# Kernel optimization log

Hardware: AMD Instinct MI355X
Metric: run time of the kernel (lower is better)

## Reference

```python
import jax, jax.numpy as jnp
import numpy as np

N_NODES = 50000
N_EDGES = 800000
D_IN = 7
H = 64
STEPS = 3


def _mlp(x, Ws, bs, act):
    n = len(Ws)
    for i in range(n):
        x = x @ Ws[i] + bs[i]
        if i < n - 1:
            x = act(x)
    return x


def _layer_norm(x, scale, bias, eps=1e-6):
    mu = jnp.mean(x, axis=-1, keepdims=True)
    var = jnp.var(x, axis=-1, keepdims=True)
    return (x - mu) * jax.lax.rsqrt(var + eps) * scale + bias


def setup_inputs() -> dict:
    key = jax.random.key(0)
    ks = jax.random.split(key, 32)

    def w(k, shape):
        fan_in = shape[-2] if len(shape) >= 2 else 1
        return jax.random.normal(k, shape, dtype=jnp.float32) / np.sqrt(fan_in)

    inp = {}
    inp["nodes"] = jax.random.normal(ks[0], (N_NODES, D_IN), dtype=jnp.float32)
    inp["senders"] = jax.random.randint(ks[1], (N_EDGES,), 0, N_NODES, dtype=jnp.int32)
    inp["receivers"] = jax.random.randint(ks[2], (N_EDGES,), 0, N_NODES, dtype=jnp.int32)

    inp["W_emb"] = w(ks[3], (D_IN, H))
    inp["b_emb"] = jnp.zeros((H,), jnp.float32)

    # edge MLPs: step 0 first layer sees concat(senders, receivers) = 2H,
    # steps 1,2 see concat(edges, senders, receivers) = 3H; hidden layers H->H
    inp["eW0_first"] = w(ks[4], (2 * H, H))
    inp["eW0_rest"] = w(ks[5], (2, 3 * H, H))
    inp["eW_hid"] = w(ks[6], (STEPS, 2, H, H))
    inp["eb"] = jnp.zeros((STEPS, 3, H), jnp.float32)

    # node MLPs: first layer sees concat(nodes, received) = 2H every step
    inp["nW0"] = w(ks[7], (STEPS, 2 * H, H))
    inp["nW_hid"] = w(ks[8], (STEPS, 2, H, H))
    inp["nb"] = jnp.zeros((STEPS, 3, H), jnp.float32)

    # layer norms per step (nodes and edges)
    inp["ln_ns"] = jnp.ones((STEPS, H), jnp.float32)
    inp["ln_nb"] = jnp.zeros((STEPS, H), jnp.float32)
    inp["ln_es"] = jnp.ones((STEPS, H), jnp.float32)
    inp["ln_eb"] = jnp.zeros((STEPS, H), jnp.float32)

    # readout MLP widths: [4*H, 2*H, 2*H, 1]
    inp["rW1"] = w(ks[9], (H, 4 * H))
    inp["rb1"] = jnp.zeros((4 * H,), jnp.float32)
    inp["rW2"] = w(ks[10], (4 * H, 2 * H))
    inp["rb2"] = jnp.zeros((2 * H,), jnp.float32)
    inp["rW3"] = w(ks[11], (2 * H, 2 * H))
    inp["rb3"] = jnp.zeros((2 * H,), jnp.float32)
    inp["rW4"] = w(ks[12], (2 * H, 1))
    inp["rb4"] = jnp.zeros((1,), jnp.float32)
    return inp


def reference(nodes, senders, receivers, W_emb, b_emb, eW0_first, eW0_rest,
              eW_hid, eb, nW0, nW_hid, nb, ln_ns, ln_nb, ln_es, ln_eb,
              rW1, rb1, rW2, rb2, rW3, rb3, rW4, rb4):
    act = jax.nn.gelu
    x = nodes @ W_emb + b_emb  # [N, H] initial embedding
    edges = None
    for s in range(STEPS):
        sent = x[senders]      # [E, H] gather
        recv = x[receivers]    # [E, H] gather
        if edges is None:
            e_in = jnp.concatenate([sent, recv], axis=1)          # [E, 2H]
            W0 = eW0_first
        else:
            e_in = jnp.concatenate([edges, sent, recv], axis=1)   # [E, 3H]
            W0 = eW0_rest[s - 1]
        edges = _mlp(e_in, [W0, eW_hid[s, 0], eW_hid[s, 1]],
                     [eb[s, 0], eb[s, 1], eb[s, 2]], act)         # [E, H]
        # aggregate edge messages to receiving nodes (segment_sum scatter)
        received = jax.ops.segment_sum(edges, receivers, num_segments=N_NODES)
        n_in = jnp.concatenate([x, received], axis=1)             # [N, 2H]
        x = _mlp(n_in, [nW0[s], nW_hid[s, 0], nW_hid[s, 1]],
                 [nb[s, 0], nb[s, 1], nb[s, 2]], act)             # [N, H]
        x = _layer_norm(x, ln_ns[s], ln_nb[s])
        edges = _layer_norm(edges, ln_es[s], ln_eb[s])
    agg = jnp.mean(x, axis=0)  # graph readout, [H]
    out = _mlp(agg, [rW1, rW2, rW3, rW4], [rb1, rb2, rb3, rb4], act)  # [1]
    return out
```

## Files before the change

### kernel.cpp

```cpp
#include <hip/hip_runtime.h>
#include <hip/hip_bf16.h>


typedef unsigned short ushort;
typedef unsigned int uint;
using bf16x8 = __attribute__((ext_vector_type(8))) short;
using f32x4 = __attribute__((ext_vector_type(4))) float;

__device__ __forceinline__ f32x4 mfma16(bf16x8 a, bf16x8 b, f32x4 c) {
    return __builtin_amdgcn_mfma_f32_16x16x32_bf16(a, b, c, 0, 0, 0);
}

__device__ __forceinline__ ushort f2bf(float x) {
    union { float f; uint u; } v;
    v.f = x;
    uint r = v.u + 0x7fffu + ((v.u >> 16) & 1u);
    return (ushort)(r >> 16);
}
__device__ __forceinline__ float bf2f(ushort u) {
    union { uint u; float f; } v;
    v.u = ((uint)u) << 16;
    return v.f;
}

__device__ __forceinline__ float gelu(float x) {
    float x3 = x * x * x;
    return 0.5f * x * (1.f + tanhf(0.7978845608028654f * (x + 0.044715f * x3)));
}

__device__ __forceinline__ float wave_ln(float v, float lns, float lnb) {
    float s1 = v, s2 = v * v;
#pragma unroll
    for (int m = 32; m; m >>= 1) {
        s1 += __shfl_xor(s1, m, 64);
        s2 += __shfl_xor(s2, m, 64);
    }
    float mu = s1 * (1.f / 64.f);
    float var = s2 * (1.f / 64.f) - mu * mu;
    return (v - mu) * rsqrtf(var + 1e-6f) * lns + lnb;
}

__global__ void k_prep(const float* __restrict__ W, ushort* __restrict__ dh,
                       ushort* __restrict__ dm, ushort* __restrict__ dl,
                       int K) {
    int tid = blockIdx.x * 256 + threadIdx.x;
    if (tid >= K * 64) return;
    int j = tid & 7;
    int lane = (tid >> 3) & 63;
    int hb = (tid >> 9) & 3;
    int kc = tid >> 11;
    int k = kc * 32 + 8 * (lane >> 4) + j;
    int h = hb * 16 + (lane & 15);
    float x = W[k * 64 + h];
    ushort uh = f2bf(x);
    float r = x - bf2f(uh);
    ushort um = f2bf(r);
    float r2 = r - bf2f(um);
    ushort ul = f2bf(r2);
    dh[tid] = uh;
    dm[tid] = um;
    dl[tid] = ul;
}

template <int KC>
__device__ __forceinline__ void mfma_layer(const float* Asrc, int pad,
                                           const ushort* __restrict__ Bh,
                                           const ushort* __restrict__ Bm,
                                           const ushort* __restrict__ Bl,
                                           int lane, f32x4 acc[4]) {
    int e15 = lane & 15, l4 = lane >> 4;
#pragma unroll
    for (int kc = 0; kc < KC; ++kc) {
        const float4* ap =
            reinterpret_cast<const float4*>(Asrc + e15 * pad + kc * 32 + 8 * l4);
        float4 q0 = ap[0];
        float4 q1 = ap[1];
        float av[8] = {q0.x, q0.y, q0.z, q0.w, q1.x, q1.y, q1.z, q1.w};
        bf16x8 ah, am, al;
#pragma unroll
        for (int j = 0; j < 8; ++j) {
            float v = av[j];
            ushort h = f2bf(v);
            float r = v - bf2f(h);
            ushort m = f2bf(r);
            float r2 = r - bf2f(m);
            ushort l = f2bf(r2);
            ah[j] = (short)h;
            am[j] = (short)m;
            al[j] = (short)l;
        }
#pragma unroll
        for (int hb = 0; hb < 4; ++hb) {
            int bi = ((kc * 4 + hb) * 64 + lane) * 8;
            bf16x8 bh_ = *reinterpret_cast<const bf16x8*>(Bh + bi);
            bf16x8 bm_ = *reinterpret_cast<const bf16x8*>(Bm + bi);
            bf16x8 bl_ = *reinterpret_cast<const bf16x8*>(Bl + bi);
            acc[hb] = mfma16(ah, bh_, acc[hb]);
            acc[hb] = mfma16(ah, bm_, acc[hb]);
            acc[hb] = mfma16(am, bh_, acc[hb]);
            acc[hb] = mfma16(ah, bl_, acc[hb]);
            acc[hb] = mfma16(am, bm_, acc[hb]);
            acc[hb] = mfma16(al, bh_, acc[hb]);
        }
    }
}

template <int KIN>
__global__ __launch_bounds__(256) void k_edge_mfma(
    const float* __restrict__ x, float* __restrict__ eraw,
    const int* __restrict__ senders, const int* __restrict__ receivers,
    const ushort* __restrict__ B0h, const ushort* __restrict__ B0m,
    const ushort* __restrict__ B0l, const ushort* __restrict__ B1h,
    const ushort* __restrict__ B1m, const ushort* __restrict__ B1l,
    const ushort* __restrict__ B2h, const ushort* __restrict__ B2m,
    const ushort* __restrict__ B2l, const float* __restrict__ b0,
    const float* __restrict__ b1, const float* __restrict__ b2,
    const float* __restrict__ lnp_s, const float* __restrict__ lnp_b,
    int n_edges) {
    constexpr int KC0 = KIN / 32;
    constexpr int PAD0 = KIN + 8;
    constexpr int PAD1 = 72;
    __shared__ float As[4][16 * PAD0];
    __shared__ float Aa[4][16 * PAD1];
    int tid = threadIdx.x;
    int lane = tid & 63;
    int wsub = tid >> 6;
    float* Aw = As[wsub];
    float* Av = Aa[wsub];
    int e15 = lane & 15, l4 = lane >> 4;

    float plns = 0.f, plnb = 0.f;
    if constexpr (KIN == 192) {
        plns = lnp_s[lane];
        plnb = lnp_b[lane];
    }
    float bv0[4], bv1[4], bv2[4];
#pragma unroll
    for (int hb = 0; hb < 4; ++hb) {
        bv0[hb] = b0[hb * 16 + e15];
        bv1[hb] = b1[hb * 16 + e15];
        bv2[hb] = b2[hb * 16 + e15];
    }

    int wid = blockIdx.x * 4 + wsub;
    int nw = gridDim.x * 4;
    int ntiles = (n_edges + 15) >> 4;

    for (int t = wid; t < ntiles; t += nw) {
        int base = t << 4;
        for (int i = 0; i < 16; ++i) {
            int e = base + i;
            if (e < n_edges) {
                int snd = senders[e];
                int rcv = receivers[e];
                float s = x[(size_t)snd * 64 + lane];
                float r = x[(size_t)rcv * 64 + lane];
                if constexpr (KIN == 192) {
                    float p = wave_ln(eraw[(size_t)e * 64 + lane], plns, plnb);
                    Aw[i * PAD0 + lane] = p;
                    Aw[i * PAD0 + 64 + lane] = s;
                    Aw[i * PAD0 + 128 + lane] = r;
                } else {
                    Aw[i * PAD0 + lane] = s;
                    Aw[i * PAD0 + 64 + lane] = r;
                }
            }
        }
        f32x4 acc[4];
#pragma unroll
        for (int hb = 0; hb < 4; ++hb)
            acc[hb] = (f32x4){bv0[hb], bv0[hb], bv0[hb], bv0[hb]};
        mfma_layer<KC0>(Aw, PAD0, B0h, B0m, B0l, lane, acc);
#pragma unroll
        for (int hb = 0; hb < 4; ++hb)
#pragma unroll
            for (int r = 0; r < 4; ++r)
                Av[(4 * l4 + r) * PAD1 + hb * 16 + e15] = gelu(acc[hb][r]);
#pragma unroll
        for (int hb = 0; hb < 4; ++hb)
            acc[hb] = (f32x4){bv1[hb], bv1[hb], bv1[hb], bv1[hb]};
        mfma_layer<2>(Av, PAD1, B1h, B1m, B1l, lane, acc);
#pragma unroll
        for (int hb = 0; hb < 4; ++hb)
#pragma unroll
            for (int r = 0; r < 4; ++r)
                Av[(4 * l4 + r) * PAD1 + hb * 16 + e15] = gelu(acc[hb][r]);
#pragma unroll
        for (int hb = 0; hb < 4; ++hb)
            acc[hb] = (f32x4){bv2[hb], bv2[hb], bv2[hb], bv2[hb]};
        mfma_layer<2>(Av, PAD1, B2h, B2m, B2l, lane, acc);
#pragma unroll
        for (int hb = 0; hb < 4; ++hb)
#pragma unroll
            for (int r = 0; r < 4; ++r) {
                int e = base + 4 * l4 + r;
                if (e < n_edges)
                    eraw[(size_t)e * 64 + hb * 16 + e15] = acc[hb][r];
            }
    }
}

__global__ __launch_bounds__(256) void k_node_mfma(
    const float* __restrict__ x, const float* __restrict__ eraw,
    const int* __restrict__ row_start, const int* __restrict__ elist,
    const ushort* __restrict__ B0h, const ushort* __restrict__ B0m,
    const ushort* __restrict__ B0l, const ushort* __restrict__ B1h,
    const ushort* __restrict__ B1m, const ushort* __restrict__ B1l,
    const ushort* __restrict__ B2h, const ushort* __restrict__ B2m,
    const ushort* __restrict__ B2l, const float* __restrict__ b0,
    const float* __restrict__ b1, const float* __restrict__ b2,
    const float* __restrict__ ln_s, const float* __restrict__ ln_b,
    float* __restrict__ xout, int n) {
    constexpr int PAD0 = 136;
    constexpr int PAD1 = 72;
    __shared__ float As[4][16 * PAD0];
    __shared__ float Aa[4][16 * PAD1];
    int tid = threadIdx.x;
    int lane = tid & 63;
    int wsub = tid >> 6;
    float* Aw = As[wsub];
    float* Av = Aa[wsub];
    int e15 = lane & 15, l4 = lane >> 4;

    float bv0[4], bv1[4], bv2[4], lnsv[4], lnbv[4];
#pragma unroll
    for (int hb = 0; hb < 4; ++hb) {
        bv0[hb] = b0[hb * 16 + e15];
        bv1[hb] = b1[hb * 16 + e15];
        bv2[hb] = b2[hb * 16 + e15];
        lnsv[hb] = ln_s[hb * 16 + e15];
        lnbv[hb] = ln_b[hb * 16 + e15];
    }

    int wid = blockIdx.x * 4 + wsub;
    int nw = gridDim.x * 4;
    int ntiles = (n + 15) >> 4;

    for (int t = wid; t < ntiles; t += nw) {
        int base = t << 4;
        for (int i = 0; i < 16; ++i) {
            int v = base + i;
            if (v < n) {
                float xv = x[(size_t)v * 64 + lane];
                int i0 = row_start[v], i1 = row_start[v + 1];
                float rv = 0.f, rv2 = 0.f;
                int ii = i0;
                for (; ii + 1 < i1; ii += 2) {
                    rv += eraw[(size_t)elist[ii] * 64 + lane];
                    rv2 += eraw[(size_t)elist[ii + 1] * 64 + lane];
                }
                if (ii < i1) rv += eraw[(size_t)elist[ii] * 64 + lane];
                rv += rv2;
                Aw[i * PAD0 + lane] = xv;
                Aw[i * PAD0 + 64 + lane] = rv;
            }
        }
        f32x4 acc[4];
#pragma unroll
        for (int hb = 0; hb < 4; ++hb)
            acc[hb] = (f32x4){bv0[hb], bv0[hb], bv0[hb], bv0[hb]};
        mfma_layer<4>(Aw, PAD0, B0h, B0m, B0l, lane, acc);
#pragma unroll
        for (int hb = 0; hb < 4; ++hb)
#pragma unroll
            for (int r = 0; r < 4; ++r)
                Av[(4 * l4 + r) * PAD1 + hb * 16 + e15] = gelu(acc[hb][r]);
#pragma unroll
        for (int hb = 0; hb < 4; ++hb)
            acc[hb] = (f32x4){bv1[hb], bv1[hb], bv1[hb], bv1[hb]};
        mfma_layer<2>(Av, PAD1, B1h, B1m, B1l, lane, acc);
#pragma unroll
        for (int hb = 0; hb < 4; ++hb)
#pragma unroll
            for (int r = 0; r < 4; ++r)
                Av[(4 * l4 + r) * PAD1 + hb * 16 + e15] = gelu(acc[hb][r]);
#pragma unroll
        for (int hb = 0; hb < 4; ++hb)
            acc[hb] = (f32x4){bv2[hb], bv2[hb], bv2[hb], bv2[hb]};
        mfma_layer<2>(Av, PAD1, B2h, B2m, B2l, lane, acc);
        float s1[4] = {0.f, 0.f, 0.f, 0.f}, s2[4] = {0.f, 0.f, 0.f, 0.f};
#pragma unroll
        for (int hb = 0; hb < 4; ++hb)
#pragma unroll
            for (int r = 0; r < 4; ++r) {
                float vv = acc[hb][r];
                s1[r] += vv;
                s2[r] += vv * vv;
            }
#pragma unroll
        for (int m = 1; m <= 8; m <<= 1)
#pragma unroll
            for (int r = 0; r < 4; ++r) {
                s1[r] += __shfl_xor(s1[r], m, 64);
                s2[r] += __shfl_xor(s2[r], m, 64);
            }
#pragma unroll
        for (int r = 0; r < 4; ++r) {
            int v = base + 4 * l4 + r;
            if (v < n) {
                float mu = s1[r] * (1.f / 64.f);
                float var = s2[r] * (1.f / 64.f) - mu * mu;
                float rs = rsqrtf(var + 1e-6f);
#pragma unroll
                for (int hb = 0; hb < 4; ++hb)
                    xout[(size_t)v * 64 + hb * 16 + e15] =
                        (acc[hb][r] - mu) * rs * lnsv[hb] + lnbv[hb];
            }
        }
    }
}

__global__ void k_hist(const int* __restrict__ receivers, int* __restrict__ cnt,
                       int nE) {
    int e = blockIdx.x * blockDim.x + threadIdx.x;
    if (e < nE) atomicAdd(&cnt[receivers[e]], 1);
}

__global__ void k_scan1(const int* __restrict__ cnt, int* __restrict__ bsum,
                        int n) {
    __shared__ int sb[256];
    int t = threadIdx.x;
    int i = blockIdx.x * 256 + t;
    sb[t] = (i < n) ? cnt[i] : 0;
    __syncthreads();
    for (int off = 128; off; off >>= 1) {
        if (t < off) sb[t] += sb[t + off];
        __syncthreads();
    }
    if (t == 0) bsum[blockIdx.x] = sb[0];
}

__global__ void k_scan2(int* __restrict__ bsum, int nb) {
    __shared__ int sb[256];
    int t = threadIdx.x;
    int v = (t < nb) ? bsum[t] : 0;
    sb[t] = v;
    __syncthreads();
    for (int off = 1; off < 256; off <<= 1) {
        int add = (t >= off) ? sb[t - off] : 0;
        __syncthreads();
        sb[t] += add;
        __syncthreads();
    }
    if (t < nb) bsum[t] = sb[t] - v;
}

__global__ void k_scan3(const int* __restrict__ cnt, const int* __restrict__ bsum,
                        int* __restrict__ row_start, int* __restrict__ cursor,
                        int n, int nE) {
    __shared__ int sb[256];
    int t = threadIdx.x;
    int i = blockIdx.x * 256 + t;
    int v = (i < n) ? cnt[i] : 0;
    sb[t] = v;
    __syncthreads();
    for (int off = 1; off < 256; off <<= 1) {
        int add = (t >= off) ? sb[t - off] : 0;
        __syncthreads();
        sb[t] += add;
        __syncthreads();
    }
    if (i < n) {
        int ex = bsum[blockIdx.x] + sb[t] - v;
        row_start[i] = ex;
        cursor[i] = ex;
    }
    if (i == n - 1) row_start[n] = nE;
}

__global__ void k_fill(const int* __restrict__ receivers, int* __restrict__ cursor,
                       int* __restrict__ elist, int nE) {
    int e = blockIdx.x * blockDim.x + threadIdx.x;
    if (e < nE) {
        int r = receivers[e];
        int p = atomicAdd(&cursor[r], 1);
        elist[p] = e;
    }
}

__global__ void k_embed(const float* __restrict__ nodes,
                        const float* __restrict__ W, const float* __restrict__ b,
                        float* __restrict__ x, int n) {
    int lane = threadIdx.x & 63;
    int wid = blockIdx.x * 4 + (threadIdx.x >> 6);
    int nw = gridDim.x * 4;
    float wcol[7];
#pragma unroll
    for (int k = 0; k < 7; ++k) wcol[k] = W[k * 64 + lane];
    float bh = b[lane];
    for (int v = wid; v < n; v += nw) {
        float acc = bh;
#pragma unroll
        for (int k = 0; k < 7; ++k) acc = fmaf(nodes[v * 7 + k], wcol[k], acc);
        x[(size_t)v * 64 + lane] = acc;
    }
}

__global__ void k_mean(const float* __restrict__ x, float* __restrict__ agg,
                       int n) {
    int t = threadIdx.x;
    int h = t & 63;
    int sub = t >> 6;
    float s = 0.f;
    for (int v = blockIdx.x * 4 + sub; v < n; v += gridDim.x * 4)
        s += x[(size_t)v * 64 + h];
    __shared__ float buf[256];
    buf[t] = s;
    __syncthreads();
    if (t < 64) {
        float tot = buf[t] + buf[t + 64] + buf[t + 128] + buf[t + 192];
        atomicAdd(&agg[h], tot);
    }
}

__global__ void k_readout(const float* __restrict__ agg,
                          const float* __restrict__ W1, const float* __restrict__ b1,
                          const float* __restrict__ W2, const float* __restrict__ b2,
                          const float* __restrict__ W3, const float* __restrict__ b3,
                          const float* __restrict__ W4, const float* __restrict__ b4,
                          float* __restrict__ out, float inv_n) {
    __shared__ float sA[64], sH1[256], sH2[128], sH3[128];
    int t = threadIdx.x;
    if (t < 64) sA[t] = agg[t] * inv_n;
    __syncthreads();
    {
        float acc = b1[t];
#pragma unroll
        for (int k = 0; k < 64; ++k) acc = fmaf(sA[k], W1[k * 256 + t], acc);
        sH1[t] = gelu(acc);
    }
    __syncthreads();
    if (t < 128) {
        float acc = b2[t];
        for (int k = 0; k < 256; ++k) acc = fmaf(sH1[k], W2[k * 128 + t], acc);
        sH2[t] = gelu(acc);
    }
    __syncthreads();
    if (t < 128) {
        float acc = b3[t];
        for (int k = 0; k < 128; ++k) acc = fmaf(sH2[k], W3[k * 128 + t], acc);
        sH3[t] = gelu(acc);
    }
    __syncthreads();
    if (t < 64) {
        float p = fmaf(sH3[t], W4[t], sH3[t + 64] * W4[t + 64]);
#pragma unroll
        for (int m = 32; m; m >>= 1) p += __shfl_xor(p, m, 64);
        if (t == 0) out[0] = p + b4[0];
    }
}

extern "C" void kernel_launch(void* const* d_in, const int* in_sizes, int n_in,
                              void* d_out, int out_size, void* d_ws,
                              size_t ws_size, hipStream_t stream) {
    const float* nodes = (const float*)d_in[0];
    const int* senders = (const int*)d_in[1];
    const int* receivers = (const int*)d_in[2];
    const float* W_emb = (const float*)d_in[3];
    const float* b_emb = (const float*)d_in[4];
    const float* eW0_first = (const float*)d_in[5];
    const float* eW0_rest = (const float*)d_in[6];
    const float* eW_hid = (const float*)d_in[7];
    const float* eb = (const float*)d_in[8];
    const float* nW0 = (const float*)d_in[9];
    const float* nW_hid = (const float*)d_in[10];
    const float* nb = (const float*)d_in[11];
    const float* ln_ns = (const float*)d_in[12];
    const float* ln_nb = (const float*)d_in[13];
    const float* ln_es = (const float*)d_in[14];
    const float* ln_eb = (const float*)d_in[15];
    const float* rW1 = (const float*)d_in[16];
    const float* rb1 = (const float*)d_in[17];
    const float* rW2 = (const float*)d_in[18];
    const float* rb2 = (const float*)d_in[19];
    const float* rW3 = (const float*)d_in[20];
    const float* rb3 = (const float*)d_in[21];
    const float* rW4 = (const float*)d_in[22];
    const float* rb4 = (const float*)d_in[23];

    const int N = in_sizes[0] / 7;
    const int E = in_sizes[1];

    float* ws = (float*)d_ws;
    float* eraw = ws;
    float* xa = eraw + (size_t)E * 64;
    float* xb = xa + (size_t)N * 64;
    float* agg = xb + (size_t)N * 64;
    int* cnt = (int*)(agg + 64);
    int* row_start = cnt + N;
    int* cursor = row_start + N + 1;
    int* elist = cursor + N;
    int* bsum = elist + E;
    const int WTOT = 106496;
    ushort* wfh = (ushort*)(bsum + 256);
    ushort* wfm = wfh + WTOT;
    ushort* wfl = wfm + WTOT;

    const int OFF_E0 = 0;
    const int OFF_E1 = 8192;
    const int OFF_E2 = 20480;
    const int OFF_EH = 32768;
    const int OFF_N0 = 57344;
    const int OFF_NH = 81920;

    k_prep<<<32, 256, 0, stream>>>(eW0_first, wfh + OFF_E0, wfm + OFF_E0,
                                   wfl + OFF_E0, 128);
    k_prep<<<48, 256, 0, stream>>>(eW0_rest, wfh + OFF_E1, wfm + OFF_E1,
                                   wfl + OFF_E1, 192);
    k_prep<<<48, 256, 0, stream>>>(eW0_rest + (size_t)192 * 64, wfh + OFF_E2,
                                   wfm + OFF_E2, wfl + OFF_E2, 192);
    for (int i = 0; i < 6; ++i) {
        k_prep<<<16, 256, 0, stream>>>(eW_hid + (size_t)i * 4096,
                                       wfh + OFF_EH + i * 4096,
                                       wfm + OFF_EH + i * 4096,
                                       wfl + OFF_EH + i * 4096, 64);
        k_prep<<<16, 256, 0, stream>>>(nW_hid + (size_t)i * 4096,
                                       wfh + OFF_NH + i * 4096,
                                       wfm + OFF_NH + i * 4096,
                                       wfl + OFF_NH + i * 4096, 64);
    }
    for (int s = 0; s < 3; ++s)
        k_prep<<<32, 256, 0, stream>>>(nW0 + (size_t)s * 8192,
                                       wfh + OFF_N0 + s * 8192,
                                       wfm + OFF_N0 + s * 8192,
                                       wfl + OFF_N0 + s * 8192, 128);

    const int nb_scan = (N + 255) / 256;

    hipMemsetAsync(cnt, 0, (size_t)N * sizeof(int), stream);
    k_hist<<<(E + 255) / 256, 256, 0, stream>>>(receivers, cnt, E);
    k_scan1<<<nb_scan, 256, 0, stream>>>(cnt, bsum, N);
    k_scan2<<<1, 256, 0, stream>>>(bsum, nb_scan);
    k_scan3<<<nb_scan, 256, 0, stream>>>(cnt, bsum, row_start, cursor, N, E);
    k_fill<<<(E + 255) / 256, 256, 0, stream>>>(receivers, cursor, elist, E);

    k_embed<<<512, 256, 0, stream>>>(nodes, W_emb, b_emb, xa, N);

    float* xc = xa;
    float* xn = xb;
    for (int s = 0; s < 3; ++s) {
        int h1 = OFF_EH + (s * 2 + 0) * 4096;
        int h2 = OFF_EH + (s * 2 + 1) * 4096;
        const float* eb0 = eb + (s * 3 + 0) * 64;
        const float* eb1 = eb + (s * 3 + 1) * 64;
        const float* eb2 = eb + (s * 3 + 2) * 64;
        if (s == 0) {
            k_edge_mfma<128><<<1024, 256, 0, stream>>>(
                xc, eraw, senders, receivers, wfh + OFF_E0, wfm + OFF_E0,
                wfl + OFF_E0, wfh + h1, wfm + h1, wfl + h1, wfh + h2, wfm + h2,
                wfl + h2, eb0, eb1, eb2, nullptr, nullptr, E);
        } else {
            int w0 = (s == 1) ? OFF_E1 : OFF_E2;
            k_edge_mfma<192><<<1024, 256, 0, stream>>>(
                xc, eraw, senders, receivers, wfh + w0, wfm + w0, wfl + w0,
                wfh + h1, wfm + h1, wfl + h1, wfh + h2, wfm + h2, wfl + h2,
                eb0, eb1, eb2, ln_es + (s - 1) * 64, ln_eb + (s - 1) * 64, E);
        }
        int n1 = OFF_NH + (s * 2 + 0) * 4096;
        int n2 = OFF_NH + (s * 2 + 1) * 4096;
        int n0 = OFF_N0 + s * 8192;
        k_node_mfma<<<512, 256, 0, stream>>>(
            xc, eraw, row_start, elist, wfh + n0, wfm + n0, wfl + n0, wfh + n1,
            wfm + n1, wfl + n1, wfh + n2, wfm + n2, wfl + n2,
            nb + (s * 3 + 0) * 64, nb + (s * 3 + 1) * 64, nb + (s * 3 + 2) * 64,
            ln_ns + s * 64, ln_nb + s * 64, xn, N);
        float* tmp = xc;
        xc = xn;
        xn = tmp;
    }

    hipMemsetAsync(agg, 0, 64 * sizeof(float), stream);
    k_mean<<<256, 256, 0, stream>>>(xc, agg, N);
    k_readout<<<1, 256, 0, stream>>>(agg, rW1, rb1, rW2, rb2, rW3, rb3, rW4,
                                     rb4, (float*)d_out, 1.0f / (float)N);
}
```

Baseline: 4.220 ms.

## Store activations pre-split into bf16 hi/mid/lo triples in global and LDS

Node features are now written once as a three-way bf16 split (a packed hi/mid uint plus a lo ushort) by the embed and node kernels. The edge kernel gathers these pre-split values, and both MLP kernels keep their LDS activation tiles as three bf16 planes. This moves the fp32-to-triple-bf16 splitting out of the MFMA inner loop and avoids re-splitting the gathered sender/receiver rows for every edge. In exchange each gathered element costs 6 bytes instead of 4, LDS traffic grows and is done with 16-bit stores, and the node state is now updated in place instead of ping-ponged between two buffers.

```diff
diff --git a/kernel.cpp b/kernel.cpp
--- a/kernel.cpp
+++ b/kernel.cpp
@@ -63,32 +63,17 @@
 }
 
 template <int KC>
-__device__ __forceinline__ void mfma_layer(const float* Asrc, int pad,
-                                           const ushort* __restrict__ Bh,
-                                           const ushort* __restrict__ Bm,
-                                           const ushort* __restrict__ Bl,
-                                           int lane, f32x4 acc[4]) {
+__device__ __forceinline__ void mfma_layer_p(
+    const ushort* Ah, const ushort* Am, const ushort* Al, int pad,
+    const ushort* __restrict__ Bh, const ushort* __restrict__ Bm,
+    const ushort* __restrict__ Bl, int lane, f32x4 acc[4]) {
     int e15 = lane & 15, l4 = lane >> 4;
 #pragma unroll
     for (int kc = 0; kc < KC; ++kc) {
-        const float4* ap =
-            reinterpret_cast<const float4*>(Asrc + e15 * pad + kc * 32 + 8 * l4);
-        float4 q0 = ap[0];
-        float4 q1 = ap[1];
-        float av[8] = {q0.x, q0.y, q0.z, q0.w, q1.x, q1.y, q1.z, q1.w};
-        bf16x8 ah, am, al;
-#pragma unroll
-        for (int j = 0; j < 8; ++j) {
-            float v = av[j];
-            ushort h = f2bf(v);
-            float r = v - bf2f(h);
-            ushort m = f2bf(r);
-            float r2 = r - bf2f(m);
-            ushort l = f2bf(r2);
-            ah[j] = (short)h;
-            am[j] = (short)m;
-            al[j] = (short)l;
-        }
+        int ao = e15 * pad + kc * 32 + 8 * l4;
+        bf16x8 ah = *reinterpret_cast<const bf16x8*>(Ah + ao);
+        bf16x8 am = *reinterpret_cast<const bf16x8*>(Am + ao);
+        bf16x8 al = *reinterpret_cast<const bf16x8*>(Al + ao);
 #pragma unroll
         for (int hb = 0; hb < 4; ++hb) {
             int bi = ((kc * 4 + hb) * 64 + lane) * 8;
@@ -107,26 +92,27 @@
 
 template <int KIN>
 __global__ __launch_bounds__(256) void k_edge_mfma(
-    const float* __restrict__ x, float* __restrict__ eraw,
-    const int* __restrict__ senders, const int* __restrict__ receivers,
-    const ushort* __restrict__ B0h, const ushort* __restrict__ B0m,
-    const ushort* __restrict__ B0l, const ushort* __restrict__ B1h,
-    const ushort* __restrict__ B1m, const ushort* __restrict__ B1l,
-    const ushort* __restrict__ B2h, const ushort* __restrict__ B2m,
-    const ushort* __restrict__ B2l, const float* __restrict__ b0,
-    const float* __restrict__ b1, const float* __restrict__ b2,
-    const float* __restrict__ lnp_s, const float* __restrict__ lnp_b,
-    int n_edges) {
+    const uint* __restrict__ xhm, const ushort* __restrict__ xl,
+    float* __restrict__ eraw, const int* __restrict__ senders,
+    const int* __restrict__ receivers, const ushort* __restrict__ B0h,
+    const ushort* __restrict__ B0m, const ushort* __restrict__ B0l,
+    const ushort* __restrict__ B1h, const ushort* __restrict__ B1m,
+    const ushort* __restrict__ B1l, const ushort* __restrict__ B2h,
+    const ushort* __restrict__ B2m, const ushort* __restrict__ B2l,
+    const float* __restrict__ b0, const float* __restrict__ b1,
+    const float* __restrict__ b2, const float* __restrict__ lnp_s,
+    const float* __restrict__ lnp_b, int n_edges) {
     constexpr int KC0 = KIN / 32;
-    constexpr int PAD0 = KIN + 8;
-    constexpr int PAD1 = 72;
-    __shared__ float As[4][16 * PAD0];
-    __shared__ float Aa[4][16 * PAD1];
+    constexpr int PAD = KIN + 8;
+    __shared__ ushort Ah[4][16 * PAD];
+    __shared__ ushort Am[4][16 * PAD];
+    __shared__ ushort Al[4][16 * PAD];
     int tid = threadIdx.x;
     int lane = tid & 63;
     int wsub = tid >> 6;
-    float* Aw = As[wsub];
-    float* Av = Aa[wsub];
+    ushort* ah_ = Ah[wsub];
+    ushort* am_ = Am[wsub];
+    ushort* al_ = Al[wsub];
     int e15 = lane & 15, l4 = lane >> 4;
 
     float plns = 0.f, plnb = 0.f;
@@ -153,16 +139,33 @@
             if (e < n_edges) {
                 int snd = senders[e];
                 int rcv = receivers[e];
-                float s = x[(size_t)snd * 64 + lane];
-                float r = x[(size_t)rcv * 64 + lane];
+                uint shm = xhm[(size_t)snd * 64 + lane];
+                ushort sl = xl[(size_t)snd * 64 + lane];
+                uint rhm = xhm[(size_t)rcv * 64 + lane];
+                ushort rl = xl[(size_t)rcv * 64 + lane];
+                int o = i * PAD;
                 if constexpr (KIN == 192) {
                     float p = wave_ln(eraw[(size_t)e * 64 + lane], plns, plnb);
-                    Aw[i * PAD0 + lane] = p;
-                    Aw[i * PAD0 + 64 + lane] = s;
-                    Aw[i * PAD0 + 128 + lane] = r;
+                    ushort ph = f2bf(p);
+                    float pr = p - bf2f(ph);
+                    ushort pm = f2bf(pr);
+                    ushort pl = f2bf(pr - bf2f(pm));
+                    ah_[o + lane] = ph;
+                    am_[o + lane] = pm;
+                    al_[o + lane] = pl;
+                    ah_[o + 64 + lane] = (ushort)(shm & 0xffffu);
+                    am_[o + 64 + lane] = (ushort)(shm >> 16);
+                    al_[o + 64 + lane] = sl;
+                    ah_[o + 128 + lane] = (ushort)(rhm & 0xffffu);
+                    am_[o + 128 + lane] = (ushort)(rhm >> 16);
+                    al_[o + 128 + lane] = rl;
                 } else {
-                    Aw[i * PAD0 + lane] = s;
-                    Aw[i * PAD0 + 64 + lane] = r;
+                    ah_[o + lane] = (ushort)(shm & 0xffffu);
+                    am_[o + lane] = (ushort)(shm >> 16);
+                    al_[o + lane] = sl;
+                    ah_[o + 64 + lane] = (ushort)(rhm & 0xffffu);
+                    am_[o + 64 + lane] = (ushort)(rhm >> 16);
+                    al_[o + 64 + lane] = rl;
                 }
             }
         }
@@ -170,25 +173,43 @@
 #pragma unroll
         for (int hb = 0; hb < 4; ++hb)
             acc[hb] = (f32x4){bv0[hb], bv0[hb], bv0[hb], bv0[hb]};
-        mfma_layer<KC0>(Aw, PAD0, B0h, B0m, B0l, lane, acc);
-#pragma unroll
-        for (int hb = 0; hb < 4; ++hb)
-#pragma unroll
-            for (int r = 0; r < 4; ++r)
-                Av[(4 * l4 + r) * PAD1 + hb * 16 + e15] = gelu(acc[hb][r]);
+        mfma_layer_p<KC0>(ah_, am_, al_, PAD, B0h, B0m, B0l, lane, acc);
+#pragma unroll
+        for (int hb = 0; hb < 4; ++hb)
+#pragma unroll
+            for (int r = 0; r < 4; ++r) {
+                float v = gelu(acc[hb][r]);
+                ushort vh = f2bf(v);
+                float vr = v - bf2f(vh);
+                ushort vm = f2bf(vr);
+                ushort vl = f2bf(vr - bf2f(vm));
+                int o = (4 * l4 + r) * PAD + hb * 16 + e15;
+                ah_[o] = vh;
+                am_[o] = vm;
+                al_[o] = vl;
+            }
 #pragma unroll
         for (int hb = 0; hb < 4; ++hb)
             acc[hb] = (f32x4){bv1[hb], bv1[hb], bv1[hb], bv1[hb]};
-        mfma_layer<2>(Av, PAD1, B1h, B1m, B1l, lane, acc);
-#pragma unroll
-        for (int hb = 0; hb < 4; ++hb)
-#pragma unroll
-            for (int r = 0; r < 4; ++r)
-                Av[(4 * l4 + r) * PAD1 + hb * 16 + e15] = gelu(acc[hb][r]);
+        mfma_layer_p<2>(ah_, am_, al_, PAD, B1h, B1m, B1l, lane, acc);
+#pragma unroll
+        for (int hb = 0; hb < 4; ++hb)
+#pragma unroll
+            for (int r = 0; r < 4; ++r) {
+                float v = gelu(acc[hb][r]);
+                ushort vh = f2bf(v);
+                float vr = v - bf2f(vh);
+                ushort vm = f2bf(vr);
+                ushort vl = f2bf(vr - bf2f(vm));
+                int o = (4 * l4 + r) * PAD + hb * 16 + e15;
+                ah_[o] = vh;
+                am_[o] = vm;
+                al_[o] = vl;
+            }
 #pragma unroll
         for (int hb = 0; hb < 4; ++hb)
             acc[hb] = (f32x4){bv2[hb], bv2[hb], bv2[hb], bv2[hb]};
-        mfma_layer<2>(Av, PAD1, B2h, B2m, B2l, lane, acc);
+        mfma_layer_p<2>(ah_, am_, al_, PAD, B2h, B2m, B2l, lane, acc);
 #pragma unroll
         for (int hb = 0; hb < 4; ++hb)
 #pragma unroll
@@ -201,25 +222,26 @@
 }
 
 __global__ __launch_bounds__(256) void k_node_mfma(
-    const float* __restrict__ x, const float* __restrict__ eraw,
-    const int* __restrict__ row_start, const int* __restrict__ elist,
-    const ushort* __restrict__ B0h, const ushort* __restrict__ B0m,
-    const ushort* __restrict__ B0l, const ushort* __restrict__ B1h,
-    const ushort* __restrict__ B1m, const ushort* __restrict__ B1l,
-    const ushort* __restrict__ B2h, const ushort* __restrict__ B2m,
-    const ushort* __restrict__ B2l, const float* __restrict__ b0,
-    const float* __restrict__ b1, const float* __restrict__ b2,
-    const float* __restrict__ ln_s, const float* __restrict__ ln_b,
-    float* __restrict__ xout, int n) {
-    constexpr int PAD0 = 136;
-    constexpr int PAD1 = 72;
-    __shared__ float As[4][16 * PAD0];
-    __shared__ float Aa[4][16 * PAD1];
+    float* __restrict__ x, uint* __restrict__ xhm, ushort* __restrict__ xl,
+    const float* __restrict__ eraw, const int* __restrict__ row_start,
+    const int* __restrict__ elist, const ushort* __restrict__ B0h,
+    const ushort* __restrict__ B0m, const ushort* __restrict__ B0l,
+    const ushort* __restrict__ B1h, const ushort* __restrict__ B1m,
+    const ushort* __restrict__ B1l, const ushort* __restrict__ B2h,
+    const ushort* __restrict__ B2m, const ushort* __restrict__ B2l,
+    const float* __restrict__ b0, const float* __restrict__ b1,
+    const float* __restrict__ b2, const float* __restrict__ ln_s,
+    const float* __restrict__ ln_b, int n) {
+    constexpr int PAD = 136;
+    __shared__ ushort Ah[4][16 * PAD];
+    __shared__ ushort Am[4][16 * PAD];
+    __shared__ ushort Al[4][16 * PAD];
     int tid = threadIdx.x;
     int lane = tid & 63;
     int wsub = tid >> 6;
-    float* Aw = As[wsub];
-    float* Av = Aa[wsub];
+    ushort* ah_ = Ah[wsub];
+    ushort* am_ = Am[wsub];
+    ushort* al_ = Al[wsub];
     int e15 = lane & 15, l4 = lane >> 4;
 
     float bv0[4], bv1[4], bv2[4], lnsv[4], lnbv[4];
@@ -241,7 +263,12 @@
         for (int i = 0; i < 16; ++i) {
             int v = base + i;
             if (v < n) {
-                float xv = x[(size_t)v * 64 + lane];
+                uint hm = xhm[(size_t)v * 64 + lane];
+                ushort lo = xl[(size_t)v * 64 + lane];
+                int o = i * PAD;
+                ah_[o + lane] = (ushort)(hm & 0xffffu);
+                am_[o + lane] = (ushort)(hm >> 16);
+                al_[o + lane] = lo;
                 int i0 = row_start[v], i1 = row_start[v + 1];
                 float rv = 0.f, rv2 = 0.f;
                 int ii = i0;
@@ -251,33 +278,56 @@
                 }
                 if (ii < i1) rv += eraw[(size_t)elist[ii] * 64 + lane];
                 rv += rv2;
-                Aw[i * PAD0 + lane] = xv;
-                Aw[i * PAD0 + 64 + lane] = rv;
+                ushort rh = f2bf(rv);
+                float rr = rv - bf2f(rh);
+                ushort rm = f2bf(rr);
+                ushort rl = f2bf(rr - bf2f(rm));
+                ah_[o + 64 + lane] = rh;
+                am_[o + 64 + lane] = rm;
+                al_[o + 64 + lane] = rl;
             }
         }
         f32x4 acc[4];
 #pragma unroll
         for (int hb = 0; hb < 4; ++hb)
             acc[hb] = (f32x4){bv0[hb], bv0[hb], bv0[hb], bv0[hb]};
-        mfma_layer<4>(Aw, PAD0, B0h, B0m, B0l, lane, acc);
-#pragma unroll
-        for (int hb = 0; hb < 4; ++hb)
-#pragma unroll
-            for (int r = 0; r < 4; ++r)
-                Av[(4 * l4 + r) * PAD1 + hb * 16 + e15] = gelu(acc[hb][r]);
+        mfma_layer_p<4>(ah_, am_, al_, PAD, B0h, B0m, B0l, lane, acc);
+#pragma unroll
+        for (int hb = 0; hb < 4; ++hb)
+#pragma unroll
+            for (int r = 0; r < 4; ++r) {
+                float v = gelu(acc[hb][r]);
+                ushort vh = f2bf(v);
+                float vr = v - bf2f(vh);
+                ushort vm = f2bf(vr);
+                ushort vl = f2bf(vr - bf2f(vm));
+                int o = (4 * l4 + r) * PAD + hb * 16 + e15;
+                ah_[o] = vh;
+                am_[o] = vm;
+                al_[o] = vl;
+            }
 #pragma unroll
         for (int hb = 0; hb < 4; ++hb)
             acc[hb] = (f32x4){bv1[hb], bv1[hb], bv1[hb], bv1[hb]};
-        mfma_layer<2>(Av, PAD1, B1h, B1m, B1l, lane, acc);
-#pragma unroll
-        for (int hb = 0; hb < 4; ++hb)
-#pragma unroll
-            for (int r = 0; r < 4; ++r)
-                Av[(4 * l4 + r) * PAD1 + hb * 16 + e15] = gelu(acc[hb][r]);
+        mfma_layer_p<2>(ah_, am_, al_, PAD, B1h, B1m, B1l, lane, acc);
+#pragma unroll
+        for (int hb = 0; hb < 4; ++hb)
+#pragma unroll
+            for (int r = 0; r < 4; ++r) {
+                float v = gelu(acc[hb][r]);
+                ushort vh = f2bf(v);
+                float vr = v - bf2f(vh);
+                ushort vm = f2bf(vr);
+                ushort vl = f2bf(vr - bf2f(vm));
+                int o = (4 * l4 + r) * PAD + hb * 16 + e15;
+                ah_[o] = vh;
+                am_[o] = vm;
+                al_[o] = vl;
+            }
 #pragma unroll
         for (int hb = 0; hb < 4; ++hb)
             acc[hb] = (f32x4){bv2[hb], bv2[hb], bv2[hb], bv2[hb]};
-        mfma_layer<2>(Av, PAD1, B2h, B2m, B2l, lane, acc);
+        mfma_layer_p<2>(ah_, am_, al_, PAD, B2h, B2m, B2l, lane, acc);
         float s1[4] = {0.f, 0.f, 0.f, 0.f}, s2[4] = {0.f, 0.f, 0.f, 0.f};
 #pragma unroll
         for (int hb = 0; hb < 4; ++hb)
@@ -302,9 +352,17 @@
                 float var = s2[r] * (1.f / 64.f) - mu * mu;
                 float rs = rsqrtf(var + 1e-6f);
 #pragma unroll
-                for (int hb = 0; hb < 4; ++hb)
-                    xout[(size_t)v * 64 + hb * 16 + e15] =
-                        (acc[hb][r] - mu) * rs * lnsv[hb] + lnbv[hb];
+                for (int hb = 0; hb < 4; ++hb) {
+                    float y = (acc[hb][r] - mu) * rs * lnsv[hb] + lnbv[hb];
+                    size_t idx = (size_t)v * 64 + hb * 16 + e15;
+                    x[idx] = y;
+                    ushort yh = f2bf(y);
+                    float yr = y - bf2f(yh);
+                    ushort ym = f2bf(yr);
+                    ushort yl2 = f2bf(yr - bf2f(ym));
+                    xhm[idx] = (uint)yh | ((uint)ym << 16);
+                    xl[idx] = yl2;
+                }
             }
         }
     }
@@ -380,7 +438,8 @@
 
 __global__ void k_embed(const float* __restrict__ nodes,
                         const float* __restrict__ W, const float* __restrict__ b,
-                        float* __restrict__ x, int n) {
+                        float* __restrict__ x, uint* __restrict__ xhm,
+                        ushort* __restrict__ xl, int n) {
     int lane = threadIdx.x & 63;
     int wid = blockIdx.x * 4 + (threadIdx.x >> 6);
     int nw = gridDim.x * 4;
@@ -392,7 +451,14 @@
         float acc = bh;
 #pragma unroll
         for (int k = 0; k < 7; ++k) acc = fmaf(nodes[v * 7 + k], wcol[k], acc);
-        x[(size_t)v * 64 + lane] = acc;
+        size_t idx = (size_t)v * 64 + lane;
+        x[idx] = acc;
+        ushort h = f2bf(acc);
+        float r = acc - bf2f(h);
+        ushort m = f2bf(r);
+        ushort l = f2bf(r - bf2f(m));
+        xhm[idx] = (uint)h | ((uint)m << 16);
+        xl[idx] = l;
     }
 }
 
@@ -483,9 +549,8 @@
 
     float* ws = (float*)d_ws;
     float* eraw = ws;
-    float* xa = eraw + (size_t)E * 64;
-    float* xb = xa + (size_t)N * 64;
-    float* agg = xb + (size_t)N * 64;
+    float* x = eraw + (size_t)E * 64;
+    float* agg = x + (size_t)N * 64;
     int* cnt = (int*)(agg + 64);
     int* row_start = cnt + N;
     int* cursor = row_start + N + 1;
@@ -495,6 +560,8 @@
     ushort* wfh = (ushort*)(bsum + 256);
     ushort* wfm = wfh + WTOT;
     ushort* wfl = wfm + WTOT;
+    uint* xhm = (uint*)(wfl + WTOT);
+    ushort* xl = (ushort*)(xhm + (size_t)N * 64);
 
     const int OFF_E0 = 0;
     const int OFF_E1 = 8192;
@@ -534,10 +601,8 @@
     k_scan3<<<nb_scan, 256, 0, stream>>>(cnt, bsum, row_start, cursor, N, E);
     k_fill<<<(E + 255) / 256, 256, 0, stream>>>(receivers, cursor, elist, E);
 
-    k_embed<<<512, 256, 0, stream>>>(nodes, W_emb, b_emb, xa, N);
-
-    float* xc = xa;
-    float* xn = xb;
+    k_embed<<<512, 256, 0, stream>>>(nodes, W_emb, b_emb, x, xhm, xl, N);
+
     for (int s = 0; s < 3; ++s) {
         int h1 = OFF_EH + (s * 2 + 0) * 4096;
         int h2 = OFF_EH + (s * 2 + 1) * 4096;
@@ -546,31 +611,29 @@
         const float* eb2 = eb + (s * 3 + 2) * 64;
         if (s == 0) {
             k_edge_mfma<128><<<1024, 256, 0, stream>>>(
-                xc, eraw, senders, receivers, wfh + OFF_E0, wfm + OFF_E0,
+                xhm, xl, eraw, senders, receivers, wfh + OFF_E0, wfm + OFF_E0,
                 wfl + OFF_E0, wfh + h1, wfm + h1, wfl + h1, wfh + h2, wfm + h2,
                 wfl + h2, eb0, eb1, eb2, nullptr, nullptr, E);
         } else {
             int w0 = (s == 1) ? OFF_E1 : OFF_E2;
             k_edge_mfma<192><<<1024, 256, 0, stream>>>(
-                xc, eraw, senders, receivers, wfh + w0, wfm + w0, wfl + w0,
-                wfh + h1, wfm + h1, wfl + h1, wfh + h2, wfm + h2, wfl + h2,
-                eb0, eb1, eb2, ln_es + (s - 1) * 64, ln_eb + (s - 1) * 64, E);
+                xhm, xl, eraw, senders, receivers, wfh + w0, wfm + w0,
+                wfl + w0, wfh + h1, wfm + h1, wfl + h1, wfh + h2, wfm + h2,
+                wfl + h2, eb0, eb1, eb2, ln_es + (s - 1) * 64,
+                ln_eb + (s - 1) * 64, E);
         }
         int n1 = OFF_NH + (s * 2 + 0) * 4096;
         int n2 = OFF_NH + (s * 2 + 1) * 4096;
         int n0 = OFF_N0 + s * 8192;
         k_node_mfma<<<512, 256, 0, stream>>>(
-            xc, eraw, row_start, elist, wfh + n0, wfm + n0, wfl + n0, wfh + n1,
-            wfm + n1, wfl + n1, wfh + n2, wfm + n2, wfl + n2,
+            x, xhm, xl, eraw, row_start, elist, wfh + n0, wfm + n0, wfl + n0,
+            wfh + n1, wfm + n1, wfl + n1, wfh + n2, wfm + n2, wfl + n2,
             nb + (s * 3 + 0) * 64, nb + (s * 3 + 1) * 64, nb + (s * 3 + 2) * 64,
-            ln_ns + s * 64, ln_nb + s * 64, xn, N);
-        float* tmp = xc;
-        xc = xn;
-        xn = tmp;
+            ln_ns + s * 64, ln_nb + s * 64, N);
     }
 
     hipMemsetAsync(agg, 0, 64 * sizeof(float), stream);
-    k_mean<<<256, 256, 0, stream>>>(xc, agg, N);
+    k_mean<<<256, 256, 0, stream>>>(x, agg, N);
     k_readout<<<1, 256, 0, stream>>>(agg, rW1, rb1, rW2, rb2, rW3, rb3, rW4,
                                      rb4, (float*)d_out, 1.0f / (float)N);
 }
```

Measured after the change: 4.261 ms. About the same (+1.0%).
